# Kernel tuning notes

Hardware: AMD Instinct MI355X
Metric: run time of the kernel (lower is better)

Reference implementation:

```python
import jax, jax.numpy as jnp
import numpy as np
from jax import lax

EPS = 1e-5

def binarize(x):
    # sign() forward, straight-through (identity) backward, like BinarizeConv2d's .data trick
    return x + lax.stop_gradient(jnp.sign(x) - x)

def conv_nchw(x, w, stride, pad):
    return lax.conv_general_dilated(
        x, w, window_strides=(stride, stride), padding=((pad, pad), (pad, pad)),
        dimension_numbers=('NCHW', 'OIHW', 'NCHW'))

def batchnorm_train(x, gamma, beta):
    # training-mode BN: per-channel batch mean / biased variance over (N,H,W)
    mean = jnp.mean(x, axis=(0, 2, 3), keepdims=True)
    var = jnp.mean((x - mean) ** 2, axis=(0, 2, 3), keepdims=True)
    xhat = (x - mean) * lax.rsqrt(var + EPS)
    return xhat * gamma[None, :, None, None] + beta[None, :, None, None]

def hardtanh(x):
    return jnp.clip(x, -1.0, 1.0)

def setup_inputs() -> dict:
    key = jax.random.key(0)
    ks = jax.random.split(key, 7)
    N, Cin, Cout, H, W = 32, 64, 64, 128, 128
    x = jax.random.normal(ks[0], (N, Cin, H, W), dtype=jnp.float32)
    w1 = jax.random.normal(ks[1], (Cout, Cin, 3, 3), dtype=jnp.float32) * 0.05
    w2 = jax.random.normal(ks[2], (Cout, Cout, 3, 3), dtype=jnp.float32) * 0.05
    g1 = jnp.ones((Cout,), dtype=jnp.float32)
    b1 = jnp.zeros((Cout,), dtype=jnp.float32)
    g2 = jnp.ones((Cout,), dtype=jnp.float32)
    b2 = jnp.zeros((Cout,), dtype=jnp.float32)
    return {"x": x, "w1": w1, "g1": g1, "b1": b1, "w2": w2, "g2": g2, "b2": b2}

def reference(x, w1, g1, b1, w2, g2, b2):
    # conv1: binarized input (C=64 != 3) and binarized weights
    out = conv_nchw(binarize(x), binarize(w1), stride=1, pad=1)
    out = hardtanh(batchnorm_train(out, g1, b1))
    # conv2: 3x3, stride 1 (stride==1 branch)
    out = conv_nchw(binarize(out), binarize(w2), stride=1, pad=1)
    out = batchnorm_train(out, g2, b2)
    # identity shortcut (stride==1 and in_planes==planes)
    out = out + x
    return hardtanh(out)
```

## Files before the change

### kernel.cpp

```cpp
#include <hip/hip_runtime.h>
#include <stdint.h>

typedef unsigned long long u64;
typedef unsigned int u32;

#define Nn 32
#define Cc 64
#define Hh 128
#define Ww 128
#define HPAD 130
#define WPAD 130
#define NHW_TOT (Nn*Hh*Ww)
#define NBIN 8

__global__ __launch_bounds__(256) void pack_x_kernel(const float* __restrict__ x,
                                                     u64* __restrict__ xpad) {
    int tid = threadIdx.x;
    int wp = tid & 63;
    int r = tid >> 6;
    int row = blockIdx.x * 4 + r;
    int n = row >> 7, h = row & 127;
    const float2* xp = (const float2*)(x + ((size_t)(n * Cc) * Hh + h) * Ww) + wp;
    u32 lo0 = 0, hi0 = 0, lo1 = 0, hi1 = 0;
    #pragma unroll
    for (int c = 0; c < 32; ++c) {
        float2 v = xp[c * (Hh * Ww / 2)];
        lo0 |= (__float_as_uint(v.x) >> 31) << c;
        lo1 |= (__float_as_uint(v.y) >> 31) << c;
    }
    #pragma unroll
    for (int c = 32; c < 64; ++c) {
        float2 v = xp[c * (Hh * Ww / 2)];
        hi0 |= (__float_as_uint(v.x) >> 31) << (c - 32);
        hi1 |= (__float_as_uint(v.y) >> 31) << (c - 32);
    }
    u64* dst = xpad + ((size_t)n * HPAD + h + 1) * WPAD + 2 * wp + 1;
    dst[0] = ((u64)hi0 << 32) | lo0;
    dst[1] = ((u64)hi1 << 32) | lo1;
}

__global__ __launch_bounds__(576) void pack_w_kernel(
        const float* __restrict__ w1, const float* __restrict__ w2,
        u64* __restrict__ w1b, u64* __restrict__ w2b) {
    int t = threadIdx.x;
    const float* src = blockIdx.x ? w2 : w1;
    u64* db = blockIdx.x ? w2b : w1b;
    int co = t / 9, tap = t - co * 9;
    const float* p = src + (size_t)co * 576 + tap;
    u32 lo = 0, hi = 0;
    #pragma unroll
    for (int ci = 0; ci < 32; ++ci)
        lo |= (__float_as_uint(p[ci * 9]) >> 31) << ci;
    #pragma unroll
    for (int ci = 32; ci < 64; ++ci)
        hi |= (__float_as_uint(p[ci * 9]) >> 31) << (ci - 32);
    db[t] = ((u64)hi << 32) | lo;
}

__device__ __forceinline__ void conv4(const u64* __restrict__ L0, const u64* __restrict__ L1,
                                      const u64* __restrict__ L2, int w,
                                      const u64 W[9], int corrMid, int v[4]) {
    u64 a[6], b[6], c[6];
    #pragma unroll
    for (int j = 0; j < 6; ++j) { a[j] = L0[w + j]; b[j] = L1[w + j]; c[j] = L2[w + j]; }
    #pragma unroll
    for (int px = 0; px < 4; ++px) {
        int p0 = __popcll(a[px] ^ W[0]) + __popcll(a[px + 1] ^ W[1]) + __popcll(a[px + 2] ^ W[2]);
        int p1 = __popcll(b[px] ^ W[3]) + __popcll(b[px + 1] ^ W[4]) + __popcll(b[px + 2] ^ W[5]);
        int p2 = __popcll(c[px] ^ W[6]) + __popcll(c[px + 1] ^ W[7]) + __popcll(c[px + 2] ^ W[8]);
        v[px] = 576 - 2 * (p0 + p1 + p2) - corrMid;
    }
}

struct LaneCtx {
    u64 W[9];
    int corrMid, corrW0, corrW127;
    int n, h;
};

__device__ __forceinline__ void lane_setup(LaneCtx& C, const u64* __restrict__ wb,
                                           int lane, int blk, int wv) {
    C.n = blk >> 5;
    int hb = (blk & 31) << 2;
    C.h = hb + wv;
    #pragma unroll
    for (int t = 0; t < 9; ++t) C.W[t] = wb[lane * 9 + t];
    int wc[9];
    #pragma unroll
    for (int t = 0; t < 9; ++t) wc[t] = 64 - 2 * __popcll(C.W[t]);
    int tT = wc[0] + wc[1] + wc[2], tB = wc[6] + wc[7] + wc[8];
    int tL = wc[0] + wc[3] + wc[6], tR = wc[2] + wc[5] + wc[8];
    bool fT = (C.h == 0), fB = (C.h == 127);
    C.corrMid  = (fT ? tT : 0) + (fB ? tB : 0);
    C.corrW0   = tL - (fT ? wc[0] : 0) - (fB ? wc[6] : 0);
    C.corrW127 = tR - (fT ? wc[2] : 0) - (fB ? wc[8] : 0);
}

__global__ __launch_bounds__(256) void conv_statsB(const u64* __restrict__ inpad,
        const u64* __restrict__ wb, u64* __restrict__ gsum, u64* __restrict__ gsq) {
    __shared__ u64 win[6 * 130];
    int tid = threadIdx.x;
    int lane = tid & 63;
    int wv = __builtin_amdgcn_readfirstlane(tid >> 6);
    int blk = blockIdx.x;
    int n = blk >> 5, hb = (blk & 31) << 2;
    const u64* src = inpad + ((size_t)n * HPAD + hb) * WPAD;
    for (int i = tid; i < 780; i += 256) win[i] = src[i];
    LaneCtx C;
    lane_setup(C, wb, lane, blk, wv);
    __syncthreads();
    const u64* L0 = &win[wv * 130];
    const u64* L1 = L0 + 130;
    const u64* L2 = L0 + 260;
    int s = 0, q = 0;
    for (int w = 0; w < 128; w += 4) {
        int v[4];
        conv4(L0, L1, L2, w, C.W, C.corrMid, v);
        if (w == 0)   v[0] -= C.corrW0;
        if (w == 124) v[3] -= C.corrW127;
        #pragma unroll
        for (int px = 0; px < 4; ++px) { s += v[px]; q += __mul24(v[px], v[px]); }
    }
    __syncthreads();
    int* r32 = (int*)win;
    r32[wv * 64 + lane] = s;
    r32[256 + wv * 64 + lane] = q;
    __syncthreads();
    if (wv == 0) {
        int S = r32[lane] + r32[64 + lane] + r32[128 + lane] + r32[192 + lane];
        int Q = r32[256 + lane] + r32[320 + lane] + r32[384 + lane] + r32[448 + lane];
        int bin = blk & (NBIN - 1);
        atomicAdd(&gsum[bin * 64 + lane], (u64)(long long)S);
        atomicAdd(&gsq[bin * 64 + lane], (u64)(long long)Q);
    }
}

__global__ __launch_bounds__(64) void bn_finalize_kernel(
        const u64* __restrict__ sum, const u64* __restrict__ sq,
        const float* __restrict__ g, const float* __restrict__ bet,
        float2* __restrict__ ab) {
    int c = threadIdx.x;
    long long Sv = 0, Qv = 0;
    #pragma unroll
    for (int b = 0; b < NBIN; ++b) {
        Sv += (long long)sum[b * 64 + c];
        Qv += (long long)sq[b * 64 + c];
    }
    double mean = (double)Sv / (double)NHW_TOT;
    double var = (double)Qv / (double)NHW_TOT - mean * mean;
    double invstd = 1.0 / sqrt(var + 1e-5);
    double a = (double)g[c] * invstd;
    double b_ = (double)bet[c] - a * mean;
    ab[c] = make_float2((float)a, (float)b_);
}

__global__ __launch_bounds__(256) void signpackB(const u64* __restrict__ inpad,
        const u64* __restrict__ wb, const float2* __restrict__ ab,
        u64* __restrict__ outpad) {
    __shared__ u64 win[6 * 130];
    int tid = threadIdx.x;
    int lane = tid & 63;
    int wv = __builtin_amdgcn_readfirstlane(tid >> 6);
    int blk = blockIdx.x;
    int n = blk >> 5, hb = (blk & 31) << 2;
    const u64* src = inpad + ((size_t)n * HPAD + hb) * WPAD;
    for (int i = tid; i < 780; i += 256) win[i] = src[i];
    LaneCtx C;
    lane_setup(C, wb, lane, blk, wv);
    float2 cab = ab[lane];
    float aa = cab.x, bb = cab.y;
    __syncthreads();
    const u64* L0 = &win[wv * 130];
    const u64* L1 = L0 + 130;
    const u64* L2 = L0 + 260;
    u64* drow = outpad + ((size_t)C.n * HPAD + C.h + 1) * WPAD + 1;
    for (int w = 0; w < 128; w += 4) {
        int v[4];
        conv4(L0, L1, L2, w, C.W, C.corrMid, v);
        if (w == 0)   v[0] -= C.corrW0;
        if (w == 124) v[3] -= C.corrW127;
        u64 wd[4];
        #pragma unroll
        for (int px = 0; px < 4; ++px) {
            float t = fmaf((float)v[px], aa, bb);
            wd[px] = __ballot(t < 0.0f);
        }
        if (lane == 0) {
            drow[w] = wd[0]; drow[w + 1] = wd[1]; drow[w + 2] = wd[2]; drow[w + 3] = wd[3];
        }
    }
}

__global__ __launch_bounds__(256) void finalB(const u64* __restrict__ inpad,
        const u64* __restrict__ wb, const float2* __restrict__ ab,
        const float* __restrict__ x, float* __restrict__ out) {
    __shared__ u64 win[6 * 130];
    __shared__ float tile[4][64 * 33];
    int tid = threadIdx.x;
    int lane = tid & 63;
    int wv = __builtin_amdgcn_readfirstlane(tid >> 6);
    int blk = blockIdx.x;
    int n = blk >> 5, hb = (blk & 31) << 2;
    const u64* src = inpad + ((size_t)n * HPAD + hb) * WPAD;
    for (int i = tid; i < 780; i += 256) win[i] = src[i];
    LaneCtx C;
    lane_setup(C, wb, lane, blk, wv);
    float2 cab = ab[lane];
    float aa = cab.x, bb = cab.y;
    __syncthreads();
    const u64* L0 = &win[wv * 130];
    const u64* L1 = L0 + 130;
    const u64* L2 = L0 + 260;
    float* T = tile[wv];
    int hl = lane >> 5, pix = lane & 31;
    size_t fbase = (((size_t)C.n * 64 + hl) * Hh + C.h) * Ww + pix;
    for (int w = 0; w < 128; w += 4) {
        int v[4];
        conv4(L0, L1, L2, w, C.W, C.corrMid, v);
        if (w == 0)   v[0] -= C.corrW0;
        if (w == 124) v[3] -= C.corrW127;
        #pragma unroll
        for (int px = 0; px < 4; ++px) {
            float t = fmaf((float)v[px], aa, bb);
            T[lane * 33 + ((w + px) & 31)] = t;
        }
        if ((w & 31) == 28) {
            int w0 = w & ~31;
            #pragma unroll 8
            for (int st = 0; st < 32; ++st) {
                int co = st * 2 + hl;
                size_t idx = fbase + ((size_t)st << 15) + w0;
                float y = T[co * 33 + pix] + x[idx];
                y = fminf(1.0f, fmaxf(-1.0f, y));
                out[idx] = y;
            }
        }
    }
}

extern "C" void kernel_launch(void* const* d_in, const int* in_sizes, int n_in,
                              void* d_out, int out_size, void* d_ws, size_t ws_size,
                              hipStream_t stream) {
    const float* x  = (const float*)d_in[0];
    const float* w1 = (const float*)d_in[1];
    const float* g1 = (const float*)d_in[2];
    const float* b1 = (const float*)d_in[3];
    const float* w2 = (const float*)d_in[4];
    const float* g2 = (const float*)d_in[5];
    const float* b2 = (const float*)d_in[6];
    float* out = (float*)d_out;
    char* ws = (char*)d_ws;

    constexpr size_t SZ_PAD   = (size_t)Nn * HPAD * WPAD * sizeof(u64);
    constexpr size_t OFF_YPAD = SZ_PAD;
    constexpr size_t OFF_W1B  = 2 * SZ_PAD;
    constexpr size_t OFF_W2B  = OFF_W1B + 576 * 8;
    constexpr size_t OFF_STAT = OFF_W2B + 576 * 8;
    constexpr size_t SZ_STAT  = (size_t)NBIN * 64 * 8;
    constexpr size_t OFF_AB1  = OFF_STAT + 4 * SZ_STAT;
    constexpr size_t OFF_AB2  = OFF_AB1 + 64 * 8;
    constexpr size_t WS_NEEDED = OFF_AB2 + 64 * 8;

    if (ws_size < WS_NEEDED) return;

    u64* xpad = (u64*)(ws);
    u64* ypad = (u64*)(ws + OFF_YPAD);
    u64* w1b  = (u64*)(ws + OFF_W1B);
    u64* w2b  = (u64*)(ws + OFF_W2B);
    u64* gsum1 = (u64*)(ws + OFF_STAT);
    u64* gsq1  = (u64*)(ws + OFF_STAT + SZ_STAT);
    u64* gsum2 = (u64*)(ws + OFF_STAT + 2 * SZ_STAT);
    u64* gsq2  = (u64*)(ws + OFF_STAT + 3 * SZ_STAT);
    float2* ab1 = (float2*)(ws + OFF_AB1);
    float2* ab2 = (float2*)(ws + OFF_AB2);

    hipMemsetAsync(ws, 0, 2 * SZ_PAD, stream);
    hipMemsetAsync(ws + OFF_STAT, 0, 4 * SZ_STAT, stream);

    pack_x_kernel<<<1024, 256, 0, stream>>>(x, xpad);
    pack_w_kernel<<<2, 576, 0, stream>>>(w1, w2, w1b, w2b);
    conv_statsB<<<1024, 256, 0, stream>>>(xpad, w1b, gsum1, gsq1);
    bn_finalize_kernel<<<1, 64, 0, stream>>>(gsum1, gsq1, g1, b1, ab1);
    signpackB<<<1024, 256, 0, stream>>>(xpad, w1b, ab1, ypad);
    conv_statsB<<<1024, 256, 0, stream>>>(ypad, w2b, gsum2, gsq2);
    bn_finalize_kernel<<<1, 64, 0, stream>>>(gsum2, gsq2, g2, b2, ab2);
    finalB<<<1024, 256, 0, stream>>>(ypad, w2b, ab2, x, out);
}
```

Before: 245.1 us.

## Fold BN finalize into consumers, widen x packing and output stores, optionally spill conv1 results

Removes the two single-block BN finalize launches by having every consumer block compute the per-channel scale and shift from the binned sums. The x pack kernel and the final residual/hardtanh stage now use float4 loads and stores, and the two workspace memsets are merged into one. When the workspace is large enough, conv1 writes its int16 outputs (about 67 MB) so the sign-pack pass reads them instead of recomputing the binary convolution. That trades compute for heavy extra memory traffic.

```diff
diff --git a/kernel.cpp b/kernel.cpp
--- a/kernel.cpp
+++ b/kernel.cpp
@@ -13,30 +13,51 @@
 #define NHW_TOT (Nn*Hh*Ww)
 #define NBIN 8
 
-__global__ __launch_bounds__(256) void pack_x_kernel(const float* __restrict__ x,
-                                                     u64* __restrict__ xpad) {
-    int tid = threadIdx.x;
-    int wp = tid & 63;
-    int r = tid >> 6;
-    int row = blockIdx.x * 4 + r;
+__device__ __forceinline__ float2 compute_ab(const u64* __restrict__ sum, const u64* __restrict__ sq,
+        const float* __restrict__ g, const float* __restrict__ bet, int c) {
+    long long Sv = 0, Qv = 0;
+    #pragma unroll
+    for (int b = 0; b < NBIN; ++b) {
+        Sv += (long long)sum[b * 64 + c];
+        Qv += (long long)sq[b * 64 + c];
+    }
+    double mean = (double)Sv / (double)NHW_TOT;
+    double var = (double)Qv / (double)NHW_TOT - mean * mean;
+    double invstd = 1.0 / sqrt(var + 1e-5);
+    double a = (double)g[c] * invstd;
+    double b_ = (double)bet[c] - a * mean;
+    return make_float2((float)a, (float)b_);
+}
+
+__global__ __launch_bounds__(256) void pack_x4_kernel(const float* __restrict__ x,
+                                                      u64* __restrict__ xpad) {
+    int t = blockIdx.x * 256 + threadIdx.x;
+    int P = t * 4;
+    int row = P >> 7, w0 = P & 127;
     int n = row >> 7, h = row & 127;
-    const float2* xp = (const float2*)(x + ((size_t)(n * Cc) * Hh + h) * Ww) + wp;
-    u32 lo0 = 0, hi0 = 0, lo1 = 0, hi1 = 0;
-    #pragma unroll
+    const float4* xp4 = (const float4*)(x + ((size_t)n * Cc * Hh + h) * Ww + w0);
+    u32 lo0 = 0, lo1 = 0, lo2 = 0, lo3 = 0, hi0 = 0, hi1 = 0, hi2 = 0, hi3 = 0;
+    #pragma unroll 8
     for (int c = 0; c < 32; ++c) {
-        float2 v = xp[c * (Hh * Ww / 2)];
+        float4 v = xp4[c * (Hh * Ww / 4)];
         lo0 |= (__float_as_uint(v.x) >> 31) << c;
         lo1 |= (__float_as_uint(v.y) >> 31) << c;
-    }
-    #pragma unroll
+        lo2 |= (__float_as_uint(v.z) >> 31) << c;
+        lo3 |= (__float_as_uint(v.w) >> 31) << c;
+    }
+    #pragma unroll 8
     for (int c = 32; c < 64; ++c) {
-        float2 v = xp[c * (Hh * Ww / 2)];
+        float4 v = xp4[c * (Hh * Ww / 4)];
         hi0 |= (__float_as_uint(v.x) >> 31) << (c - 32);
         hi1 |= (__float_as_uint(v.y) >> 31) << (c - 32);
-    }
-    u64* dst = xpad + ((size_t)n * HPAD + h + 1) * WPAD + 2 * wp + 1;
+        hi2 |= (__float_as_uint(v.z) >> 31) << (c - 32);
+        hi3 |= (__float_as_uint(v.w) >> 31) << (c - 32);
+    }
+    u64* dst = xpad + ((size_t)n * HPAD + h + 1) * WPAD + w0 + 1;
     dst[0] = ((u64)hi0 << 32) | lo0;
     dst[1] = ((u64)hi1 << 32) | lo1;
+    dst[2] = ((u64)hi2 << 32) | lo2;
+    dst[3] = ((u64)hi3 << 32) | lo3;
 }
 
 __global__ __launch_bounds__(576) void pack_w_kernel(
@@ -96,8 +117,10 @@
     C.corrW127 = tR - (fT ? wc[2] : 0) - (fB ? wc[8] : 0);
 }
 
-__global__ __launch_bounds__(256) void conv_statsB(const u64* __restrict__ inpad,
-        const u64* __restrict__ wb, u64* __restrict__ gsum, u64* __restrict__ gsq) {
+template<bool SPILL>
+__global__ __launch_bounds__(256) void conv_statsT(const u64* __restrict__ inpad,
+        const u64* __restrict__ wb, u64* __restrict__ gsum, u64* __restrict__ gsq,
+        short* __restrict__ v16) {
     __shared__ u64 win[6 * 130];
     int tid = threadIdx.x;
     int lane = tid & 63;
@@ -112,6 +135,7 @@
     const u64* L0 = &win[wv * 130];
     const u64* L1 = L0 + 130;
     const u64* L2 = L0 + 260;
+    short* vrow = SPILL ? (v16 + ((size_t)(C.n * Hh + C.h) * Ww) * 64 + lane) : nullptr;
     int s = 0, q = 0;
     for (int w = 0; w < 128; w += 4) {
         int v[4];
@@ -119,7 +143,11 @@
         if (w == 0)   v[0] -= C.corrW0;
         if (w == 124) v[3] -= C.corrW127;
         #pragma unroll
-        for (int px = 0; px < 4; ++px) { s += v[px]; q += __mul24(v[px], v[px]); }
+        for (int px = 0; px < 4; ++px) {
+            s += v[px];
+            q += __mul24(v[px], v[px]);
+            if (SPILL) vrow[(size_t)(w + px) * 64] = (short)v[px];
+        }
     }
     __syncthreads();
     int* r32 = (int*)win;
@@ -135,27 +163,33 @@
     }
 }
 
-__global__ __launch_bounds__(64) void bn_finalize_kernel(
+__global__ __launch_bounds__(256) void signpack_v(const short* __restrict__ v16,
         const u64* __restrict__ sum, const u64* __restrict__ sq,
         const float* __restrict__ g, const float* __restrict__ bet,
-        float2* __restrict__ ab) {
-    int c = threadIdx.x;
-    long long Sv = 0, Qv = 0;
-    #pragma unroll
-    for (int b = 0; b < NBIN; ++b) {
-        Sv += (long long)sum[b * 64 + c];
-        Qv += (long long)sq[b * 64 + c];
-    }
-    double mean = (double)Sv / (double)NHW_TOT;
-    double var = (double)Qv / (double)NHW_TOT - mean * mean;
-    double invstd = 1.0 / sqrt(var + 1e-5);
-    double a = (double)g[c] * invstd;
-    double b_ = (double)bet[c] - a * mean;
-    ab[c] = make_float2((float)a, (float)b_);
-}
-
-__global__ __launch_bounds__(256) void signpackB(const u64* __restrict__ inpad,
-        const u64* __restrict__ wb, const float2* __restrict__ ab,
+        u64* __restrict__ ypad) {
+    int tid = threadIdx.x;
+    int lane = tid & 63;
+    int wv = tid >> 6;
+    int grow = blockIdx.x * 4 + wv;
+    int n = grow >> 7, h = grow & 127;
+    float2 ab = compute_ab(sum, sq, g, bet, lane);
+    const short* vr = v16 + (size_t)grow * (Ww * 64) + lane;
+    u64* drow = ypad + ((size_t)n * HPAD + h + 1) * WPAD + 1;
+    for (int base = 0; base < 128; base += 64) {
+        u64 myw = 0;
+        #pragma unroll 8
+        for (int px = 0; px < 64; ++px) {
+            float tv = fmaf((float)vr[(size_t)(base + px) * 64], ab.x, ab.y);
+            u64 bal = __ballot(tv < 0.0f);
+            if (lane == px) myw = bal;
+        }
+        drow[base + lane] = myw;
+    }
+}
+
+__global__ __launch_bounds__(256) void signpack_rc(const u64* __restrict__ inpad,
+        const u64* __restrict__ wb, const u64* __restrict__ sum, const u64* __restrict__ sq,
+        const float* __restrict__ g, const float* __restrict__ bet,
         u64* __restrict__ outpad) {
     __shared__ u64 win[6 * 130];
     int tid = threadIdx.x;
@@ -167,8 +201,7 @@
     for (int i = tid; i < 780; i += 256) win[i] = src[i];
     LaneCtx C;
     lane_setup(C, wb, lane, blk, wv);
-    float2 cab = ab[lane];
-    float aa = cab.x, bb = cab.y;
+    float2 ab = compute_ab(sum, sq, g, bet, lane);
     __syncthreads();
     const u64* L0 = &win[wv * 130];
     const u64* L1 = L0 + 130;
@@ -182,7 +215,7 @@
         u64 wd[4];
         #pragma unroll
         for (int px = 0; px < 4; ++px) {
-            float t = fmaf((float)v[px], aa, bb);
+            float t = fmaf((float)v[px], ab.x, ab.y);
             wd[px] = __ballot(t < 0.0f);
         }
         if (lane == 0) {
@@ -191,8 +224,9 @@
     }
 }
 
-__global__ __launch_bounds__(256) void finalB(const u64* __restrict__ inpad,
-        const u64* __restrict__ wb, const float2* __restrict__ ab,
+__global__ __launch_bounds__(256) void final4_kernel(const u64* __restrict__ inpad,
+        const u64* __restrict__ wb, const u64* __restrict__ sum, const u64* __restrict__ sq,
+        const float* __restrict__ g, const float* __restrict__ bet,
         const float* __restrict__ x, float* __restrict__ out) {
     __shared__ u64 win[6 * 130];
     __shared__ float tile[4][64 * 33];
@@ -205,15 +239,16 @@
     for (int i = tid; i < 780; i += 256) win[i] = src[i];
     LaneCtx C;
     lane_setup(C, wb, lane, blk, wv);
-    float2 cab = ab[lane];
-    float aa = cab.x, bb = cab.y;
+    float2 ab = compute_ab(sum, sq, g, bet, lane);
+    float aa = ab.x, bb = ab.y;
     __syncthreads();
     const u64* L0 = &win[wv * 130];
     const u64* L1 = L0 + 130;
     const u64* L2 = L0 + 260;
     float* T = tile[wv];
-    int hl = lane >> 5, pix = lane & 31;
-    size_t fbase = (((size_t)C.n * 64 + hl) * Hh + C.h) * Ww + pix;
+    int p4 = lane & 7;
+    int cosub = lane >> 3;
+    size_t base_nch = ((size_t)C.n * Cc * Hh + C.h) * Ww;
     for (int w = 0; w < 128; w += 4) {
         int v[4];
         conv4(L0, L1, L2, w, C.W, C.corrMid, v);
@@ -227,12 +262,20 @@
         if ((w & 31) == 28) {
             int w0 = w & ~31;
             #pragma unroll 8
-            for (int st = 0; st < 32; ++st) {
-                int co = st * 2 + hl;
-                size_t idx = fbase + ((size_t)st << 15) + w0;
-                float y = T[co * 33 + pix] + x[idx];
-                y = fminf(1.0f, fmaxf(-1.0f, y));
-                out[idx] = y;
+            for (int st = 0; st < 8; ++st) {
+                int co = st * 8 + cosub;
+                size_t idx = base_nch + (size_t)co * (Hh * Ww) + w0 + p4 * 4;
+                float4 xv = *(const float4*)(x + idx);
+                float y0 = T[co * 33 + p4 * 4 + 0] + xv.x;
+                float y1 = T[co * 33 + p4 * 4 + 1] + xv.y;
+                float y2 = T[co * 33 + p4 * 4 + 2] + xv.z;
+                float y3 = T[co * 33 + p4 * 4 + 3] + xv.w;
+                float4 yv;
+                yv.x = fminf(1.0f, fmaxf(-1.0f, y0));
+                yv.y = fminf(1.0f, fmaxf(-1.0f, y1));
+                yv.z = fminf(1.0f, fmaxf(-1.0f, y2));
+                yv.w = fminf(1.0f, fmaxf(-1.0f, y3));
+                *(float4*)(out + idx) = yv;
             }
         }
     }
@@ -253,36 +296,39 @@
 
     constexpr size_t SZ_PAD   = (size_t)Nn * HPAD * WPAD * sizeof(u64);
     constexpr size_t OFF_YPAD = SZ_PAD;
-    constexpr size_t OFF_W1B  = 2 * SZ_PAD;
+    constexpr size_t OFF_STAT = 2 * SZ_PAD;
+    constexpr size_t SZ_STAT  = (size_t)NBIN * 64 * 8;
+    constexpr size_t OFF_W1B  = OFF_STAT + 4 * SZ_STAT;
     constexpr size_t OFF_W2B  = OFF_W1B + 576 * 8;
-    constexpr size_t OFF_STAT = OFF_W2B + 576 * 8;
-    constexpr size_t SZ_STAT  = (size_t)NBIN * 64 * 8;
-    constexpr size_t OFF_AB1  = OFF_STAT + 4 * SZ_STAT;
-    constexpr size_t OFF_AB2  = OFF_AB1 + 64 * 8;
-    constexpr size_t WS_NEEDED = OFF_AB2 + 64 * 8;
-
-    if (ws_size < WS_NEEDED) return;
+    constexpr size_t OFF_V16  = OFF_W2B + 576 * 8;
+    constexpr size_t SZ_V16   = (size_t)Nn * Hh * Ww * 64 * 2;
+    constexpr size_t WS_SMALL = OFF_V16;
+    constexpr size_t WS_FULL  = OFF_V16 + SZ_V16;
+
+    if (ws_size < WS_SMALL) return;
+    bool spill = (ws_size >= WS_FULL);
 
     u64* xpad = (u64*)(ws);
     u64* ypad = (u64*)(ws + OFF_YPAD);
-    u64* w1b  = (u64*)(ws + OFF_W1B);
-    u64* w2b  = (u64*)(ws + OFF_W2B);
     u64* gsum1 = (u64*)(ws + OFF_STAT);
     u64* gsq1  = (u64*)(ws + OFF_STAT + SZ_STAT);
     u64* gsum2 = (u64*)(ws + OFF_STAT + 2 * SZ_STAT);
     u64* gsq2  = (u64*)(ws + OFF_STAT + 3 * SZ_STAT);
-    float2* ab1 = (float2*)(ws + OFF_AB1);
-    float2* ab2 = (float2*)(ws + OFF_AB2);
-
-    hipMemsetAsync(ws, 0, 2 * SZ_PAD, stream);
-    hipMemsetAsync(ws + OFF_STAT, 0, 4 * SZ_STAT, stream);
-
-    pack_x_kernel<<<1024, 256, 0, stream>>>(x, xpad);
+    u64* w1b  = (u64*)(ws + OFF_W1B);
+    u64* w2b  = (u64*)(ws + OFF_W2B);
+    short* v16 = (short*)(ws + OFF_V16);
+
+    hipMemsetAsync(ws, 0, 2 * SZ_PAD + 4 * SZ_STAT, stream);
+
+    pack_x4_kernel<<<512, 256, 0, stream>>>(x, xpad);
     pack_w_kernel<<<2, 576, 0, stream>>>(w1, w2, w1b, w2b);
-    conv_statsB<<<1024, 256, 0, stream>>>(xpad, w1b, gsum1, gsq1);
-    bn_finalize_kernel<<<1, 64, 0, stream>>>(gsum1, gsq1, g1, b1, ab1);
-    signpackB<<<1024, 256, 0, stream>>>(xpad, w1b, ab1, ypad);
-    conv_statsB<<<1024, 256, 0, stream>>>(ypad, w2b, gsum2, gsq2);
-    bn_finalize_kernel<<<1, 64, 0, stream>>>(gsum2, gsq2, g2, b2, ab2);
-    finalB<<<1024, 256, 0, stream>>>(ypad, w2b, ab2, x, out);
-}
+    if (spill) {
+        conv_statsT<true><<<1024, 256, 0, stream>>>(xpad, w1b, gsum1, gsq1, v16);
+        signpack_v<<<1024, 256, 0, stream>>>(v16, gsum1, gsq1, g1, b1, ypad);
+    } else {
+        conv_statsT<false><<<1024, 256, 0, stream>>>(xpad, w1b, gsum1, gsq1, nullptr);
+        signpack_rc<<<1024, 256, 0, stream>>>(xpad, w1b, gsum1, gsq1, g1, b1, ypad);
+    }
+    conv_statsT<false><<<1024, 256, 0, stream>>>(ypad, w2b, gsum2, gsq2, nullptr);
+    final4_kernel<<<1024, 256, 0, stream>>>(ypad, w2b, gsum2, gsq2, g2, b2, x, out);
+}
```

Result: faster. 228.1 us (-7.0%).
